# Performance work log

Measured on AMD Instinct MI355X. Metric: run time of the kernel, lower is better.

The kernel has to match this reference:

```python
import jax, jax.numpy as jnp
import numpy as np
from jax import lax

GAMMA = 1.0   # soft-min temperature (init kwarg)
BIG = 1e10    # finite stand-in for +inf (safe gradients, exp(-BIG/gamma) == 0 in fp32)


def _pairwise_sqdist(X, Z):
    # X: (N, T, d), Z: (T, d) -> D: (N, T, T) squared Euclidean, without (N,T,T,d) intermediate
    x2 = jnp.sum(X * X, axis=-1)              # (N, T)
    z2 = jnp.sum(Z * Z, axis=-1)              # (T,)
    xz = jnp.einsum('ntd,sd->nts', X, Z)      # (N, T, T)
    return x2[:, :, None] + z2[None, None, :] - 2.0 * xz


def _softdtw_batch(D, gamma):
    # D: (N, T, T) cost matrices. Anti-diagonal wavefront DP:
    #   R[i,j] = D[i,j] + softmin(R[i-1,j], R[i,j-1], R[i-1,j-1]),  R[0,0]=0, borders=BIG
    # Diagonal k = i + j (i,j in 1..T); diagonal arrays indexed by ii = i-1 in [0, T).
    N, T, _ = D.shape
    ii = jnp.arange(T)
    inv_g = 1.0 / gamma

    def softmin(a, b, c):
        s = jnp.stack([a, b, c], axis=0) * (-inv_g)
        return -gamma * jax.scipy.special.logsumexp(s, axis=0)

    def step(carry, k):
        d_prev2, d_prev1 = carry              # diagonals k-2 and k-1, each (N, T)
        jj = k - 2 - ii                        # column index j-1 for row index ii
        valid = (jj >= 0) & (jj < T)
        dvals = jnp.take_along_axis(
            D, jnp.clip(jj, 0, T - 1)[None, :, None], axis=2)[..., 0]  # (N, T)
        r_left = d_prev1                                   # R[i, j-1]
        r_up = jnp.concatenate(
            [jnp.full((N, 1), BIG, D.dtype), d_prev1[:, :-1]], axis=1)  # R[i-1, j]
        corner = jnp.where(k == 2, jnp.asarray(0.0, D.dtype), jnp.asarray(BIG, D.dtype))
        r_diag = jnp.concatenate(
            [jnp.broadcast_to(corner, (N, 1)), d_prev2[:, :-1]], axis=1)  # R[i-1, j-1]
        new_d = jnp.where(valid[None, :], dvals + softmin(r_up, r_left, r_diag),
                          jnp.asarray(BIG, D.dtype))
        return (d_prev1, new_d), None

    d0 = jnp.full((N, T), BIG, D.dtype)
    (_, last), _ = lax.scan(step, (d0, d0), jnp.arange(2, 2 * T + 1))
    return last[:, T - 1]                      # R[T, T] per sample


def setup_inputs() -> dict:
    key = jax.random.key(0)
    k1, k2, k3 = jax.random.split(key, 3)
    N, T, d = 64, 512, 16
    X = jax.random.normal(k1, (N, T, d), dtype=jnp.float32)
    weights = jax.random.uniform(k2, (N,), dtype=jnp.float32)
    Z = jax.random.normal(k3, (T, d), dtype=jnp.float32)
    return {"X": X, "weights": weights, "Z": Z}


def reference(X, weights, Z):
    D = _pairwise_sqdist(X, Z)                 # (N, T, T)
    sdtw = _softdtw_batch(D, GAMMA)            # (N,)
    return jnp.sum(weights * sdtw)             # scalar barycenter loss
```

## Files before the change

kernel.cpp:

```cpp
#include <hip/hip_runtime.h>

#define TT 512
#define BIGS 1.4426950408889634e10f
#define LOG2E 1.4426950408889634f
#define M2L  (-2.0f * 1.4426950408889634f)
#define LN2F 0.69314718055994531f
#define P_SS 16
#define G_LAG 80
#define N_SS 51
#define RSTR 130

typedef _Float16 h2 __attribute__((ext_vector_type(2)));

__device__ __forceinline__ unsigned pk(float a, float b) {
    h2 v; v.x = (_Float16)a; v.y = (_Float16)b;
    return __builtin_bit_cast(unsigned, v);
}

#if __has_builtin(__builtin_amdgcn_fdot2)
#define FDOT2(a, b, c) __builtin_amdgcn_fdot2(__builtin_bit_cast(h2, (a)), \
                                              __builtin_bit_cast(h2, (b)), (c), false)
#else
__device__ __forceinline__ float fdot2_sw(unsigned a, unsigned b, float c) {
    h2 ha = __builtin_bit_cast(h2, a), hb = __builtin_bit_cast(h2, b);
    return c + (float)ha.x * (float)hb.x + (float)ha.y * (float)hb.y;
}
#define FDOT2(a, b, c) fdot2_sw((a), (b), (c))
#endif

#if __has_builtin(__builtin_amdgcn_exp2f)
#define EXP2F(x) __builtin_amdgcn_exp2f(x)
#else
#define EXP2F(x) exp2f(x)
#endif

#define ZROW(jv) (((((jv) & 1)) << 8) | ((((jv) >> 1)) & 255))

__device__ __forceinline__ float dppshr1(float x, float old) {
#if __has_builtin(__builtin_amdgcn_update_dpp)
    return __builtin_bit_cast(float,
        __builtin_amdgcn_update_dpp(__builtin_bit_cast(int, old),
                                    __builtin_bit_cast(int, x),
                                    0x138 , 0xF, 0xF, false));
#else
    const float v = __shfl_up(x, 1);
    return ((threadIdx.x & 63) == 0) ? old : v;
#endif
}

__global__ __launch_bounds__(768, 1) void k_fused(const float* __restrict__ X,
                                                  const float* __restrict__ Z,
                                                  const float* __restrict__ w,
                                                  float* __restrict__ out) {
    const int tt = threadIdx.x;
    const int t  = tt & 63;
    const int wv = tt >> 6;
    const int bd = wv & 3;
    const int hf = (wv >= 8) ? 1 : 0;
    const int n  = blockIdx.x;

    __shared__ uint4    ZA[2][512];
    __shared__ float    Zs2p[512];
    __shared__ float2   seam[4][64];
    __shared__ unsigned ring[4][64][RSTR];

    if (tt < 512) {
        const int r = tt;
        const float4* zp = (const float4*)(Z + (size_t)r * 16);
        const float4 a0 = zp[0], a1 = zp[1], a2 = zp[2], a3 = zp[3];
        float sv = 0.0f;
        sv = fmaf(a0.x, a0.x, sv); sv = fmaf(a0.y, a0.y, sv);
        sv = fmaf(a0.z, a0.z, sv); sv = fmaf(a0.w, a0.w, sv);
        sv = fmaf(a1.x, a1.x, sv); sv = fmaf(a1.y, a1.y, sv);
        sv = fmaf(a1.z, a1.z, sv); sv = fmaf(a1.w, a1.w, sv);
        sv = fmaf(a2.x, a2.x, sv); sv = fmaf(a2.y, a2.y, sv);
        sv = fmaf(a2.z, a2.z, sv); sv = fmaf(a2.w, a2.w, sv);
        sv = fmaf(a3.x, a3.x, sv); sv = fmaf(a3.y, a3.y, sv);
        sv = fmaf(a3.z, a3.z, sv); sv = fmaf(a3.w, a3.w, sv);
        const int idx = ((r & 1) << 8) | (r >> 1);
        ZA[0][idx] = make_uint4(pk(a0.x, a0.y), pk(a0.z, a0.w),
                                pk(a1.x, a1.y), pk(a1.z, a1.w));
        ZA[1][idx] = make_uint4(pk(a2.x, a2.y), pk(a2.z, a2.w),
                                pk(a3.x, a3.y), pk(a3.z, a3.w));
        Zs2p[idx] = LOG2E * sv;
    }
    if (tt < 256) ((float2*)&seam[0][0])[tt] = make_float2(BIGS, 1.0f);

    const int i0 = 128 * bd + 2 * t;
    unsigned Xu[2][8];
    float    xs2[2];
    const float* xp = X + ((size_t)n * TT + i0) * 16;
#pragma unroll
    for (int q = 0; q < 2; ++q) {
        const float4* xr = (const float4*)(xp + q * 16);
        const float4 a0 = xr[0], a1 = xr[1], a2 = xr[2], a3 = xr[3];
        float sv = 0.0f;
        sv = fmaf(a0.x, a0.x, sv); sv = fmaf(a0.y, a0.y, sv);
        sv = fmaf(a0.z, a0.z, sv); sv = fmaf(a0.w, a0.w, sv);
        sv = fmaf(a1.x, a1.x, sv); sv = fmaf(a1.y, a1.y, sv);
        sv = fmaf(a1.z, a1.z, sv); sv = fmaf(a1.w, a1.w, sv);
        sv = fmaf(a2.x, a2.x, sv); sv = fmaf(a2.y, a2.y, sv);
        sv = fmaf(a2.z, a2.z, sv); sv = fmaf(a2.w, a2.w, sv);
        sv = fmaf(a3.x, a3.x, sv); sv = fmaf(a3.y, a3.y, sv);
        sv = fmaf(a3.z, a3.z, sv); sv = fmaf(a3.w, a3.w, sv);
        xs2[q] = LOG2E * sv;
        Xu[q][0] = pk(a0.x, a0.y); Xu[q][1] = pk(a0.z, a0.w);
        Xu[q][2] = pk(a1.x, a1.y); Xu[q][3] = pk(a1.z, a1.w);
        Xu[q][4] = pk(a2.x, a2.y); Xu[q][5] = pk(a2.z, a2.w);
        Xu[q][6] = pk(a3.x, a3.y); Xu[q][7] = pk(a3.z, a3.w);
    }
    const float wgt = w[n];
    const float2* rKS = &seam[bd][0];
    unsigned* const rg = &ring[bd][t][0];
    __syncthreads();

#define PRODUCE(Tv)                                                           \
    {                                                                         \
        const int base_ = ((Tv) << 4) + (hf << 3);                            \
        const int wb_ = base_ & 127;                                          \
        _Pragma("unroll 4")                                                   \
        for (int cc = 0; cc < 8; ++cc) {                                      \
            const int zr = ZROW(base_ + cc);                \
            const uint4 z0 = ZA[0][zr], z1 = ZA[1][zr];                       \
            const float zz = Zs2p[zr];                                        \
            float a0 = 0.0f, b0 = 0.0f, a1 = 0.0f, b1 = 0.0f;                 \
            a0 = FDOT2(z0.x, Xu[0][0], a0); a0 = FDOT2(z0.y, Xu[0][1], a0);   \
            a0 = FDOT2(z0.z, Xu[0][2], a0); a0 = FDOT2(z0.w, Xu[0][3], a0);   \
            b0 = FDOT2(z1.x, Xu[0][4], b0); b0 = FDOT2(z1.y, Xu[0][5], b0);   \
            b0 = FDOT2(z1.z, Xu[0][6], b0); b0 = FDOT2(z1.w, Xu[0][7], b0);   \
            a1 = FDOT2(z0.x, Xu[1][0], a1); a1 = FDOT2(z0.y, Xu[1][1], a1);   \
            a1 = FDOT2(z0.z, Xu[1][2], a1); a1 = FDOT2(z0.w, Xu[1][3], a1);   \
            b1 = FDOT2(z1.x, Xu[1][4], b1); b1 = FDOT2(z1.y, Xu[1][5], b1);   \
            b1 = FDOT2(z1.z, Xu[1][6], b1); b1 = FDOT2(z1.w, Xu[1][7], b1);   \
            const float dd0 = fmaf(M2L, a0 + b0, xs2[0] + zz);                \
            const float dd1 = fmaf(M2L, a1 + b1, xs2[1] + zz);                \
            rg[wb_ + cc] = pk(dd0, dd1);                                      \
        }                                                                     \
    }

    if (wv >= 4 && bd == 0) { PRODUCE(0) PRODUCE(1) }
    __syncthreads();

    float RpK[2], RpS[2], poK, poS, bnK, bnS;
    unsigned rv[2];
    RpK[0] = RpK[1] = BIGS; RpS[0] = RpS[1] = 1.0f;
    poK = BIGS; poS = 1.0f; bnK = BIGS; bnS = 1.0f;
    rv[0] = rv[1] = 0u;

#define TICK(q, tl, ALLOK)                                                    \
    {                                                                         \
        const float2 sprev = rKS[((tl) + 1) & 63];        \
        const float unK = bnK, unS = bnS;                                     \
        const h2 dh = __builtin_bit_cast(h2, rv[q]);                          \
        rv[q] = rg[((unsigned)((tl) + 2 - t)) & 127];      \
        const float dd0 = (float)dh.x;                                        \
        const float dd1 = (float)dh.y;                                        \
        const float l0K = RpK[0], l0S = RpS[0];                               \
        const float m0 = fminf(fminf(unK, l0K), poK);                         \
        const float s0 = EXP2F(m0 - unK) * unS                                \
                       + EXP2F(m0 - l0K) * l0S                                \
                       + EXP2F(m0 - poK) * poS;                               \
        const float K0 = dd0 + m0;                                            \
        const float l1K = RpK[1], l1S = RpS[1];                               \
        const float m1 = fminf(fminf(K0, l1K), l0K);                          \
        const float s1 = EXP2F(m1 - K0) * s0                                  \
                       + EXP2F(m1 - l1K) * l1S                                \
                       + EXP2F(m1 - l0K) * l0S;                               \
        const float K1 = dd1 + m1;                                            \
        const int j = (tl) - t;                                               \
        const bool ok = (ALLOK) ? true : ((j >= 0) && (j < 512));             \
        RpK[0] = ok ? K0 : RpK[0];  RpS[0] = ok ? s0 : RpS[0];                \
        RpK[1] = ok ? K1 : RpK[1];  RpS[1] = ok ? s1 : RpS[1];                \
        if (ok && bd < 3 && t == 63) {                                        \
            seam[bd + 1][j & 63] = make_float2(RpK[1], RpS[1]);               \
        }                                                                     \
        poK = unK; poS = unS;                                                 \
        bnK = dppshr1(RpK[1], sprev.x);           \
        bnS = dppshr1(RpS[1], sprev.y);                                       \
    }

#define RENORM                                                                \
    {                                                                         \
        _Pragma("unroll")                                                     \
        for (int q = 0; q < 2; ++q) {                                         \
            const int e = (int)(__float_as_uint(RpS[q]) >> 23) - 127;         \
            RpS[q] = __uint_as_float(__float_as_uint(RpS[q])                  \
                                     - ((unsigned)e << 23));                  \
            RpK[q] -= (float)e;                                               \
        }                                                                     \
    }

#define SS_BODY(A)                                                            \
    TICK(0, tb + 0, A)  TICK(1, tb + 1, A)  TICK(0, tb + 2, A)                \
    TICK(1, tb + 3, A)  TICK(0, tb + 4, A)  TICK(1, tb + 5, A)                \
    TICK(0, tb + 6, A)  TICK(1, tb + 7, A)                                    \
    RENORM                                                                    \
    TICK(0, tb + 8, A)  TICK(1, tb + 9, A)  TICK(0, tb + 10, A)               \
    TICK(1, tb + 11, A) TICK(0, tb + 12, A) TICK(1, tb + 13, A)               \
    TICK(0, tb + 14, A) TICK(1, tb + 15, A)                                   \
    RENORM

#pragma unroll 1
    for (int s = 0; s < N_SS; ++s) {
        if (wv >= 4) {
            const int T = s - 5 * bd + 2;
            if (T >= 0 && T <= 31) PRODUCE(T)
        } else {
            const int tb = P_SS * s - G_LAG * bd;
            if (tb >= 64 && tb <= 496) {
                __builtin_amdgcn_s_setprio(1);
                SS_BODY(1)
                __builtin_amdgcn_s_setprio(0);
            } else if (tb >= 0 && tb <= 574) {
                if (tb == 0) {
                    RpK[0] = RpK[1] = BIGS; RpS[0] = RpS[1] = 1.0f;
                    poK = (bd == 0 && t == 0) ? 0.0f : BIGS; poS = 1.0f;
                    const float2 r0 = rKS[0];
                    bnK = r0.x; bnS = r0.y;
                    rv[0] = rg[((unsigned)(0 - t)) & 127];
                    rv[1] = rg[((unsigned)(1 - t)) & 127];
                }
                __builtin_amdgcn_s_setprio(1);
                SS_BODY(0)
                __builtin_amdgcn_s_setprio(0);
            }
        }
        __syncthreads();
    }
#undef TICK
#undef RENORM
#undef SS_BODY
#undef PRODUCE

    if (wv == 3 && t == 63) {
        atomicAdd(out, wgt * (RpK[1] - log2f(RpS[1])) * LN2F);
    }
}

__global__ void k_zero(float* out) {
    if (threadIdx.x == 0) out[0] = 0.0f;
}

extern "C" void kernel_launch(void* const* d_in, const int* in_sizes, int n_in,
                              void* d_out, int out_size, void* d_ws, size_t ws_size,
                              hipStream_t stream) {
    const float* X = (const float*)d_in[0];
    const float* w = (const float*)d_in[1];
    const float* Z = (const float*)d_in[2];
    float* out = (float*)d_out;

    hipLaunchKernelGGL(k_zero, dim3(1), dim3(64), 0, stream, out);
    hipLaunchKernelGGL(k_fused, dim3(64), dim3(768), 0, stream, X, Z, w, out);
}
```

Measured before the change: 166.7 us.

## Software-pipeline soft-DTW scale recurrence one tick behind the max-plus recurrence

Each tick now runs in two parts. It computes the min-plus K values and all six exp2 weights at once, then applies the sum-scale update from the previous tick's stored weights. Taking the exp2 latency off the serial K dependency chain should shorten the critical path of the wavefront. In exchange it adds register pressure for the E arrays and more delicate seam and boundary handling, which forces a larger inter-wave lag (G_LAG 96) and more supersteps.

```diff
diff --git a/kernel.cpp b/kernel.cpp
--- a/kernel.cpp
+++ b/kernel.cpp
@@ -6,8 +6,8 @@
 #define M2L  (-2.0f * 1.4426950408889634f)
 #define LN2F 0.69314718055994531f
 #define P_SS 16
-#define G_LAG 80
-#define N_SS 51
+#define G_LAG 96
+#define N_SS 54
 #define RSTR 130
 
 typedef _Float16 h2 __attribute__((ext_vector_type(2)));
@@ -141,42 +141,61 @@
     if (wv >= 4 && bd == 0) { PRODUCE(0) PRODUCE(1) }
     __syncthreads();
 
-    float RpK[2], RpS[2], poK, poS, bnK, bnS;
+    float RpK[2], RpS[2], poK, poS_s, bnK, bnS;
+    float E[2][6];
+    float sprevS_d;
     unsigned rv[2];
     RpK[0] = RpK[1] = BIGS; RpS[0] = RpS[1] = 1.0f;
-    poK = BIGS; poS = 1.0f; bnK = BIGS; bnS = 1.0f;
+    poK = BIGS; poS_s = 1.0f; bnK = BIGS; bnS = 1.0f;
+    sprevS_d = 1.0f;
     rv[0] = rv[1] = 0u;
-
-#define TICK(q, tl, ALLOK)                                                    \
+#pragma unroll
+    for (int e = 0; e < 6; ++e) { E[0][e] = 1.0f; E[1][e] = 1.0f; }
+
+#define LTICK(q, tl, ALLOK)                                                   \
     {                                                                         \
-        const float2 sprev = rKS[((tl) + 1) & 63];        \
-        const float unK = bnK, unS = bnS;                                     \
+        const float K1_d = RpK[1];            \
+        const float2 sprev = rKS[((tl) + 1) & 63];                            \
         const h2 dh = __builtin_bit_cast(h2, rv[q]);                          \
         rv[q] = rg[((unsigned)((tl) + 2 - t)) & 127];      \
-        const float dd0 = (float)dh.x;                                        \
-        const float dd1 = (float)dh.y;                                        \
-        const float l0K = RpK[0], l0S = RpS[0];                               \
-        const float m0 = fminf(fminf(unK, l0K), poK);                         \
-        const float s0 = EXP2F(m0 - unK) * unS                                \
-                       + EXP2F(m0 - l0K) * l0S                                \
-                       + EXP2F(m0 - poK) * poS;                               \
+        const float dd0 = (float)dh.x, dd1 = (float)dh.y;                     \
+                 \
+        const float unK = bnK;                                                \
+        const float pK  = poK;                                                \
+        const float l0K = RpK[0], l1K = RpK[1];                               \
+        const float m0 = fminf(fminf(unK, l0K), pK);                          \
         const float K0 = dd0 + m0;                                            \
-        const float l1K = RpK[1], l1S = RpS[1];                               \
         const float m1 = fminf(fminf(K0, l1K), l0K);                          \
-        const float s1 = EXP2F(m1 - K0) * s0                                  \
-                       + EXP2F(m1 - l1K) * l1S                                \
-                       + EXP2F(m1 - l0K) * l0S;                               \
         const float K1 = dd1 + m1;                                            \
-        const int j = (tl) - t;                                               \
-        const bool ok = (ALLOK) ? true : ((j >= 0) && (j < 512));             \
-        RpK[0] = ok ? K0 : RpK[0];  RpS[0] = ok ? s0 : RpS[0];                \
-        RpK[1] = ok ? K1 : RpK[1];  RpS[1] = ok ? s1 : RpS[1];                \
-        if (ok && bd < 3 && t == 63) {                                        \
-            seam[bd + 1][j & 63] = make_float2(RpK[1], RpS[1]);               \
+        const bool okK = (ALLOK) ? true                                       \
+                       : ((((tl) - t) >= 0) && (((tl) - t) < 512));           \
+        RpK[0] = okK ? K0 : RpK[0];                                           \
+        RpK[1] = okK ? K1 : RpK[1];                                           \
+        poK = unK;                                                            \
+                  \
+        E[q][0] = EXP2F(m0 - unK);                                            \
+        E[q][1] = EXP2F(m0 - l0K);                                            \
+        E[q][2] = EXP2F(m0 - pK);                                             \
+        E[q][3] = EXP2F(m1 - K0);                                             \
+        E[q][4] = EXP2F(m1 - l1K);                                            \
+        E[q][5] = EXP2F(m1 - l0K);                                            \
+          \
+        const bool okS = (ALLOK) ? true                                       \
+                       : ((((tl) - 1 - t) >= 0) && (((tl) - 1 - t) < 512));   \
+        const float s0 = E[(q) ^ 1][0] * bnS + E[(q) ^ 1][1] * RpS[0]         \
+                       + E[(q) ^ 1][2] * poS_s;                               \
+        const float s1 = E[(q) ^ 1][3] * s0 + E[(q) ^ 1][4] * RpS[1]          \
+                       + E[(q) ^ 1][5] * RpS[0];                              \
+        RpS[0] = okS ? s0 : RpS[0];                                           \
+        RpS[1] = okS ? s1 : RpS[1];                                           \
+        if (okS && bd < 3 && t == 63) {   \
+            seam[bd + 1][(tl) & 63] = make_float2(K1_d, RpS[1]);              \
         }                                                                     \
-        poK = unK; poS = unS;                                                 \
-        bnK = dppshr1(RpK[1], sprev.x);           \
-        bnS = dppshr1(RpS[1], sprev.y);                                       \
+        poS_s = bnS;                                \
+                                                 \
+        bnK = dppshr1(RpK[1], sprev.x);               \
+        bnS = dppshr1(RpS[1], sprevS_d);              \
+        sprevS_d = sprev.y;                                                   \
     }
 
 #define RENORM                                                                \
@@ -191,19 +210,19 @@
     }
 
 #define SS_BODY(A)                                                            \
-    TICK(0, tb + 0, A)  TICK(1, tb + 1, A)  TICK(0, tb + 2, A)                \
-    TICK(1, tb + 3, A)  TICK(0, tb + 4, A)  TICK(1, tb + 5, A)                \
-    TICK(0, tb + 6, A)  TICK(1, tb + 7, A)                                    \
+    LTICK(0, tb + 0, A)  LTICK(1, tb + 1, A)  LTICK(0, tb + 2, A)             \
+    LTICK(1, tb + 3, A)  LTICK(0, tb + 4, A)  LTICK(1, tb + 5, A)             \
+    LTICK(0, tb + 6, A)  LTICK(1, tb + 7, A)                                  \
     RENORM                                                                    \
-    TICK(0, tb + 8, A)  TICK(1, tb + 9, A)  TICK(0, tb + 10, A)               \
-    TICK(1, tb + 11, A) TICK(0, tb + 12, A) TICK(1, tb + 13, A)               \
-    TICK(0, tb + 14, A) TICK(1, tb + 15, A)                                   \
+    LTICK(0, tb + 8, A)  LTICK(1, tb + 9, A)  LTICK(0, tb + 10, A)            \
+    LTICK(1, tb + 11, A) LTICK(0, tb + 12, A) LTICK(1, tb + 13, A)            \
+    LTICK(0, tb + 14, A) LTICK(1, tb + 15, A)                                 \
     RENORM
 
 #pragma unroll 1
     for (int s = 0; s < N_SS; ++s) {
         if (wv >= 4) {
-            const int T = s - 5 * bd + 2;
+            const int T = s - 6 * bd + 2;
             if (T >= 0 && T <= 31) PRODUCE(T)
         } else {
             const int tb = P_SS * s - G_LAG * bd;
@@ -214,9 +233,12 @@
             } else if (tb >= 0 && tb <= 574) {
                 if (tb == 0) {
                     RpK[0] = RpK[1] = BIGS; RpS[0] = RpS[1] = 1.0f;
-                    poK = (bd == 0 && t == 0) ? 0.0f : BIGS; poS = 1.0f;
+                    poK = (bd == 0 && t == 0) ? 0.0f : BIGS;
+                    poS_s = 1.0f;
                     const float2 r0 = rKS[0];
-                    bnK = r0.x; bnS = r0.y;
+                    bnK = r0.x;
+                    bnS = 1.0f;
+                    sprevS_d = r0.y;
                     rv[0] = rg[((unsigned)(0 - t)) & 127];
                     rv[1] = rg[((unsigned)(1 - t)) & 127];
                 }
@@ -227,7 +249,7 @@
         }
         __syncthreads();
     }
-#undef TICK
+#undef LTICK
 #undef RENORM
 #undef SS_BODY
 #undef PRODUCE
```

After: 167.9 us. No clear change (+0.7%).
